# Optimization experiments

Measured on AMD Instinct MI355X. Metric: run time of the kernel, lower is better.

Reference implementation:

```python
import jax, jax.numpy as jnp
import numpy as np

NUM_HEADS = 16

def setup_inputs() -> dict:
    key = jax.random.key(0)
    k_x, k_wq, k_bq, k_wo, k_bo = jax.random.split(key, 5)
    B, S, D = 4, 2048, 1024
    x = jax.random.normal(k_x, (B, S, D), dtype=jnp.float32)
    # Flax Dense default init: lecun_normal for kernel, zeros for bias; use small normals here.
    w_qkv = jax.random.normal(k_wq, (D, 3 * D), dtype=jnp.float32) * (D ** -0.5)
    b_qkv = jnp.zeros((3 * D,), dtype=jnp.float32)
    w_out = jax.random.normal(k_wo, (D, D), dtype=jnp.float32) * (D ** -0.5)
    b_out = jnp.zeros((D,), dtype=jnp.float32)
    return {"x": x, "w_qkv": w_qkv, "b_qkv": b_qkv, "w_out": w_out, "b_out": b_out}

def reference(x, w_qkv, b_qkv, w_out, b_out):
    B, S, D = x.shape
    H = NUM_HEADS
    hd = D // H
    scale = hd ** -0.5
    qkv = x @ w_qkv + b_qkv                                  # [B,S,3D]
    qkv = qkv.reshape(B, S, 3, H, hd)
    qkv = jnp.transpose(qkv, (2, 0, 3, 1, 4))                # [3,B,H,S,hd]
    q, k, v = qkv[0], qkv[1], qkv[2]
    attn = jnp.einsum("bhqd,bhkd->bhqk", q, k) * scale       # [B,H,S,S]
    attn = jax.nn.softmax(attn, axis=-1)
    out = jnp.einsum("bhqk,bhkd->bhqd", attn, v)             # [B,H,S,hd]
    out = jnp.transpose(out, (0, 2, 1, 3)).reshape(B, S, D)
    return out @ w_out + b_out
```

## Files before the change

### kernel.cpp

```cpp
#include <hip/hip_runtime.h>
#include <cstdint>
#include <cstddef>

#define B_    4
#define S_    2048
#define D_    1024
#define H_    16
#define HD_   64
#define M_    8192
#define NQKV  3072

typedef __bf16 bf16;
typedef __bf16 bf16x4 __attribute__((ext_vector_type(4)));
typedef __bf16 bf16x8 __attribute__((ext_vector_type(8)));
typedef float  f32x2  __attribute__((ext_vector_type(2)));
typedef float  f32x4  __attribute__((ext_vector_type(4)));
typedef float  f32x16 __attribute__((ext_vector_type(16)));
typedef uint32_t u32x2 __attribute__((ext_vector_type(2)));
typedef uint32_t u32x4 __attribute__((ext_vector_type(4)));

#define MFMA16(a, b, c) __builtin_amdgcn_mfma_f32_16x16x32_bf16(a, b, c, 0, 0, 0)

__device__ __forceinline__ void gl2lds16(const void* g, void* l) {
  __builtin_amdgcn_global_load_lds(
      (__attribute__((address_space(1))) void*)(uintptr_t)g,
      (__attribute__((address_space(3))) void*)l, 16, 0, 0);
}

__device__ __forceinline__ uint32_t pkbf16(float a, float b) {
  union { bf16 h[2]; uint32_t u; } z;
  z.h[0] = (bf16)a; z.h[1] = (bf16)b;
  return z.u;
}

__global__ __launch_bounds__(256) void cast_f32_bf16(const float* __restrict__ in,
                                                     bf16* __restrict__ out, int n4) {
  int i = blockIdx.x * 256 + threadIdx.x;
  if (i >= n4) return;
  float4 v = ((const float4*)in)[i];
  bf16x4 o;
  o[0] = (bf16)v.x; o[1] = (bf16)v.y; o[2] = (bf16)v.z; o[3] = (bf16)v.w;
  ((bf16x4*)out)[i] = o;
}

__global__ __launch_bounds__(256) void transpose_cast(const float* __restrict__ in,
                                                      bf16* __restrict__ out, int R, int C) {
  __shared__ float tile[32][33];
  int bx = blockIdx.x * 32, by = blockIdx.y * 32;
  int tx = threadIdx.x, ty = threadIdx.y;
#pragma unroll
  for (int i = 0; i < 32; i += 8)
    tile[ty + i][tx] = in[(size_t)(by + ty + i) * C + bx + tx];
  __syncthreads();
#pragma unroll
  for (int i = 0; i < 32; i += 8)
    out[(size_t)(bx + ty + i) * R + by + tx] = (bf16)tile[tx][ty + i];
}

template <bool OUT_BF16>
__global__ __launch_bounds__(512, 2) void gemm256(const bf16* __restrict__ A,
                                                  const bf16* __restrict__ Bt,
                                                  const float* __restrict__ bias,
                                                  void* __restrict__ Cptr,
                                                  int M, int N, int K) {
  extern __shared__ __align__(16) bf16 sm[];
  const int tid  = threadIdx.x;
  const int lane = tid & 63, w = tid >> 6;
  const int lo   = lane & 15, quad = lane >> 4;
  const int wr   = w >> 1, wc = w & 1;
  const int xcd  = blockIdx.x & 7, g = blockIdx.x >> 3;
  const int mi_  = g & 3, n_ = g >> 2;
  const int bm   = (xcd * 4 + mi_) * 256, bn = n_ * 128;

  const bf16* Ag = A  + (size_t)bm * K;
  const bf16* Bg = Bt + (size_t)bn * K;

  const int swzl  = lo & 7;
  const int laneA = (wr * 64 + lo) * 64;
  const int laneB = (wc * 64 + lo) * 64;
  const int pc0   = (quad ^ swzl) * 8;
  const int pc1   = ((4 + quad) ^ swzl) * 8;

  int aoffG[4], boffG[2];
#pragma unroll
  for (int la = 0; la < 4; ++la) {
    int ca = la * 512 + tid, row = ca >> 3, s = ca & 7;
    aoffG[la] = row * K + ((s ^ (row & 7)) * 8);
  }
#pragma unroll
  for (int lb = 0; lb < 2; ++lb) {
    int cb = lb * 512 + tid, row = cb >> 3, s = cb & 7;
    boffG[lb] = row * K + ((s ^ (row & 7)) * 8);
  }
  const int T = K >> 6;

  f32x4 acc[4][4];
  const f32x4 zero = {0.f, 0.f, 0.f, 0.f};
#pragma unroll
  for (int i = 0; i < 4; ++i)
#pragma unroll
    for (int j = 0; j < 4; ++j) acc[i][j] = zero;

#pragma unroll
  for (int la = 0; la < 4; ++la)
    gl2lds16(Ag + aoffG[la], sm + (la * 512 + tid) * 8);
#pragma unroll
  for (int lb = 0; lb < 2; ++lb)
    gl2lds16(Bg + boffG[lb], sm + 16384 + (lb * 512 + tid) * 8);
#pragma unroll
  for (int la = 0; la < 4; ++la)
    gl2lds16(Ag + 64 + aoffG[la], sm + 24576 + (la * 512 + tid) * 8);
#pragma unroll
  for (int lb = 0; lb < 2; ++lb)
    gl2lds16(Bg + 64 + boffG[lb], sm + 24576 + 16384 + (lb * 512 + tid) * 8);
  asm volatile("s_waitcnt vmcnt(6)" ::: "memory");
  __builtin_amdgcn_s_barrier();

  auto body = [&](int t, bool st) __attribute__((always_inline)) {
    bf16* As_ = sm + (t % 3) * 24576;
    bf16* Bs_ = As_ + 16384;
    bf16* An_ = sm + ((t + 2) % 3) * 24576;
    bf16* Bn_ = An_ + 16384;
    const size_t kg = (size_t)(t + 2) * 64;
    bf16x8 av0, av1, bv[4];

    av0 = *(const bf16x8*)&As_[laneA + 0 * 1024 + pc0];
    av1 = *(const bf16x8*)&As_[laneA + 1 * 1024 + pc0];
#pragma unroll
    for (int j = 0; j < 4; ++j)
      bv[j] = *(const bf16x8*)&Bs_[laneB + j * 1024 + pc0];
    if (st) {
      gl2lds16(Ag + kg + aoffG[0], An_ + (0 * 512 + tid) * 8);
      gl2lds16(Ag + kg + aoffG[1], An_ + (1 * 512 + tid) * 8);
    }
    __builtin_amdgcn_s_barrier();
    __builtin_amdgcn_s_setprio(1);
#pragma unroll
    for (int j = 0; j < 4; ++j) {
      acc[0][j] = MFMA16(av0, bv[j], acc[0][j]);
      acc[1][j] = MFMA16(av1, bv[j], acc[1][j]);
    }
    __builtin_amdgcn_s_setprio(0);

    av0 = *(const bf16x8*)&As_[laneA + 2 * 1024 + pc0];
    av1 = *(const bf16x8*)&As_[laneA + 3 * 1024 + pc0];
    if (st) {
      gl2lds16(Ag + kg + aoffG[2], An_ + (2 * 512 + tid) * 8);
      gl2lds16(Ag + kg + aoffG[3], An_ + (3 * 512 + tid) * 8);
    }
    __builtin_amdgcn_s_barrier();
    __builtin_amdgcn_s_setprio(1);
#pragma unroll
    for (int j = 0; j < 4; ++j) {
      acc[2][j] = MFMA16(av0, bv[j], acc[2][j]);
      acc[3][j] = MFMA16(av1, bv[j], acc[3][j]);
    }
    __builtin_amdgcn_s_setprio(0);

    av0 = *(const bf16x8*)&As_[laneA + 0 * 1024 + pc1];
    av1 = *(const bf16x8*)&As_[laneA + 1 * 1024 + pc1];
#pragma unroll
    for (int j = 0; j < 4; ++j)
      bv[j] = *(const bf16x8*)&Bs_[laneB + j * 1024 + pc1];
    if (st)
      gl2lds16(Bg + kg + boffG[0], Bn_ + (0 * 512 + tid) * 8);
    __builtin_amdgcn_s_barrier();
    __builtin_amdgcn_s_setprio(1);
#pragma unroll
    for (int j = 0; j < 4; ++j) {
      acc[0][j] = MFMA16(av0, bv[j], acc[0][j]);
      acc[1][j] = MFMA16(av1, bv[j], acc[1][j]);
    }
    __builtin_amdgcn_s_setprio(0);

    av0 = *(const bf16x8*)&As_[laneA + 2 * 1024 + pc1];
    av1 = *(const bf16x8*)&As_[laneA + 3 * 1024 + pc1];
    if (st)
      gl2lds16(Bg + kg + boffG[1], Bn_ + (1 * 512 + tid) * 8);
    __builtin_amdgcn_s_barrier();
    __builtin_amdgcn_s_setprio(1);
#pragma unroll
    for (int j = 0; j < 4; ++j) {
      acc[2][j] = MFMA16(av0, bv[j], acc[2][j]);
      acc[3][j] = MFMA16(av1, bv[j], acc[3][j]);
    }
    __builtin_amdgcn_s_setprio(0);
  };

#pragma unroll 1
  for (int t = 0; t < T - 2; ++t) {
    body(t, true);
    asm volatile("s_waitcnt vmcnt(6)" ::: "memory");
    __builtin_amdgcn_s_barrier();
  }
  body(T - 2, false);
  asm volatile("s_waitcnt vmcnt(0)" ::: "memory");
  __builtin_amdgcn_s_barrier();
  body(T - 1, false);

#pragma unroll
  for (int j = 0; j < 4; ++j) {
    int cg = bn + wc * 64 + j * 16 + lo;
    float bsv = bias[cg];
#pragma unroll
    for (int i = 0; i < 4; ++i) {
      int rg = bm + wr * 64 + i * 16 + quad * 4;
#pragma unroll
      for (int r = 0; r < 4; ++r) {
        float v = acc[i][j][r] + bsv;
        if (OUT_BF16) ((bf16*)Cptr)[(size_t)(rg + r) * N + cg] = (bf16)v;
        else          ((float*)Cptr)[(size_t)(rg + r) * N + cg] = v;
      }
    }
  }
}

__global__ __launch_bounds__(256, 2) void flash_attn(const bf16* __restrict__ qkv,
                                                     bf16* __restrict__ out) {
  __shared__ __align__(16) bf16 smem[16384];
  bf16* const Ksm = smem;
  bf16* const Vsm = smem + 8192;

  const int tid  = threadIdx.x;
  const int lane = tid & 63, wq = tid >> 6;
  const int l31  = lane & 31;
  const int e    = lane >> 5;
  const int hi8  = e * 8, hi4 = e * 4;

  const int bid = blockIdx.x;
  const int qb  = bid >> 6;
  const int bh  = bid & 63;
  const int h   = bh & 15;
  const int b   = bh >> 4;
  const int q0  = qb * 256;
  const size_t rowb = (size_t)b * S_;
  const bf16* qbase = qkv + rowb * NQKV + h * HD_;
  const bf16* kbase = qbase + D_;
  const bf16* vbase = qbase + 2 * D_;

  bf16x8 qfA[4], qfB[4];
  {
    const bf16* qrow0 = qbase + (size_t)(q0 + wq * 64 + l31) * NQKV;
    const bf16* qrow1 = qrow0 + (size_t)32 * NQKV;
#pragma unroll
    for (int c = 0; c < 4; ++c) {
      qfA[c] = *(const bf16x8*)(qrow0 + c * 16 + hi8);
      qfB[c] = *(const bf16x8*)(qrow1 + c * 16 + hi8);
    }
  }

  int kq_off[2];
#pragma unroll
  for (int it = 0; it < 2; ++it) {
    int ci = it * 256 + tid;
    int s  = ci >> 3;
    int x  = (ci & 7) ^ (s & 7);
    kq_off[it] = s * NQKV + x * 8;
  }
  int vs_d[2], vs_s[2], vs_off[2];
#pragma unroll
  for (int u = 0; u < 2; ++u) {
    int idx = u * 256 + tid;
    int d0 = (idx & 31) * 2;
    int s0 = (idx >> 5) * 4;
    vs_d[u] = d0;
    vs_s[u] = s0;
    vs_off[u] = (((s0 >> 3) ^ ((d0 >> 1) & 7)) * 8) + (s0 & 7);
  }

  uint32_t vreg[2][4];

  const f32x16 zero16 = {0.f,0.f,0.f,0.f,0.f,0.f,0.f,0.f,0.f,0.f,0.f,0.f,0.f,0.f,0.f,0.f};
  f32x16 oacc[2][2];
  oacc[0][0] = zero16; oacc[0][1] = zero16;
  oacc[1][0] = zero16; oacc[1][1] = zero16;
  f32x16 sAc[2], sBc[2];
  f32x2 psA = {0.f, 0.f}, psB = {0.f, 0.f};
  const float c2 = 0.125f * 1.44269504088896341f;

#define KDMA(KT, PB) {                                                      \
    const bf16* kb_ = kbase + (size_t)(KT) * 64 * NQKV;                     \
    _Pragma("unroll")                                                       \
    for (int it = 0; it < 2; ++it)                                          \
      gl2lds16(kb_ + kq_off[it], Ksm + (PB) * 4096 + (it * 256 + wq * 64) * 8); \
  }
#define VLOAD(KT) {                                                         \
    const bf16* vb_ = vbase + (size_t)(KT) * 64 * NQKV;                     \
    _Pragma("unroll")                                                       \
    for (int u = 0; u < 2; ++u)                                             \
      _Pragma("unroll")                                                     \
      for (int j = 0; j < 4; ++j)                                           \
        vreg[u][j] = *(const uint32_t*)(vb_ + (size_t)(vs_s[u] + j) * NQKV + vs_d[u]); \
  }
#define VWRITE(PB) {                                                        \
    _Pragma("unroll")                                                       \
    for (int u = 0; u < 2; ++u) {                                           \
      int d0_ = vs_d[u];                                                    \
      uint32_t lo0 = __builtin_amdgcn_perm(vreg[u][1], vreg[u][0], 0x05040100u); \
      uint32_t lo1 = __builtin_amdgcn_perm(vreg[u][3], vreg[u][2], 0x05040100u); \
      uint32_t hi0 = __builtin_amdgcn_perm(vreg[u][1], vreg[u][0], 0x07060302u); \
      uint32_t hi1 = __builtin_amdgcn_perm(vreg[u][3], vreg[u][2], 0x07060302u); \
      u32x2 lov = {lo0, lo1}, hiv = {hi0, hi1};                             \
      *(u32x2*)&Vsm[(PB) * 4096 + (d0_ + 0) * 64 + vs_off[u]] = lov;        \
      *(u32x2*)&Vsm[(PB) * 4096 + (d0_ + 1) * 64 + vs_off[u]] = hiv;        \
    }                                                                       \
  }

  auto smfma = [&](int P) __attribute__((always_inline)) {
    sAc[0] = zero16; sBc[0] = zero16;
    sAc[1] = zero16; sBc[1] = zero16;
    __builtin_amdgcn_s_setprio(1);
#pragma unroll
    for (int c = 0; c < 4; ++c) {
#pragma unroll
      for (int kk = 0; kk < 2; ++kk) {
        int srow = kk * 32 + l31;
        int swz  = (srow & 7) * 8;
        bf16x8 kf = *(const bf16x8*)&Ksm[P * 4096 + srow * 64 + ((c * 16 + hi8) ^ swz)];
        sAc[kk] = __builtin_amdgcn_mfma_f32_32x32x16_bf16(kf, qfA[c], sAc[kk], 0, 0, 0);
        sBc[kk] = __builtin_amdgcn_mfma_f32_32x32x16_bf16(kf, qfB[c], sBc[kk], 0, 0, 0);
      }
    }
    __builtin_amdgcn_s_setprio(0);
  };

  auto softpv = [&](int P) __attribute__((always_inline)) {
#pragma unroll
    for (int kk = 0; kk < 2; ++kk) {
      uint32_t Q8a[8], Q8b[8];
#pragma unroll
      for (int i = 0; i < 8; ++i) {
        f32x2 sva, svb;
        sva[0] = sAc[kk][2 * i]; sva[1] = sAc[kk][2 * i + 1];
        svb[0] = sBc[kk][2 * i]; svb[1] = sBc[kk][2 * i + 1];
        f32x2 ta = sva * c2 - 16.0f;
        f32x2 tb = svb * c2 - 16.0f;
        float a0 = __builtin_amdgcn_exp2f(ta[0]);
        float a1 = __builtin_amdgcn_exp2f(ta[1]);
        float b0 = __builtin_amdgcn_exp2f(tb[0]);
        float b1 = __builtin_amdgcn_exp2f(tb[1]);
        psA += (f32x2){a0, a1};
        psB += (f32x2){b0, b1};
        Q8a[i] = pkbf16(a0, a1);
        Q8b[i] = pkbf16(b0, b1);
      }
#pragma unroll
      for (int mh = 0; mh < 2; ++mh) {
        const int m = kk * 2 + mh, bq = mh * 4;
        u32x4 pda, pdb;
#if __has_builtin(__builtin_amdgcn_permlane32_swap)
        u32x2 wa0 = __builtin_amdgcn_permlane32_swap(Q8a[bq],     Q8a[bq + 2], false, false);
        u32x2 wa1 = __builtin_amdgcn_permlane32_swap(Q8a[bq + 1], Q8a[bq + 3], false, false);
        pda[0] = wa0[0]; pda[1] = wa1[0]; pda[2] = wa0[1]; pda[3] = wa1[1];
        u32x2 wb0 = __builtin_amdgcn_permlane32_swap(Q8b[bq],     Q8b[bq + 2], false, false);
        u32x2 wb1 = __builtin_amdgcn_permlane32_swap(Q8b[bq + 1], Q8b[bq + 3], false, false);
        pdb[0] = wb0[0]; pdb[1] = wb1[0]; pdb[2] = wb0[1]; pdb[3] = wb1[1];
#else
        {
          uint32_t s0 = e ? Q8a[bq]     : Q8a[bq + 2];
          uint32_t s1 = e ? Q8a[bq + 1] : Q8a[bq + 3];
          uint32_t r0 = __shfl_xor(s0, 32);
          uint32_t r1 = __shfl_xor(s1, 32);
          pda[0] = e ? r0 : Q8a[bq];
          pda[1] = e ? r1 : Q8a[bq + 1];
          pda[2] = e ? Q8a[bq + 2] : r0;
          pda[3] = e ? Q8a[bq + 3] : r1;
        }
        {
          uint32_t s0 = e ? Q8b[bq]     : Q8b[bq + 2];
          uint32_t s1 = e ? Q8b[bq + 1] : Q8b[bq + 3];
          uint32_t r0 = __shfl_xor(s0, 32);
          uint32_t r1 = __shfl_xor(s1, 32);
          pdb[0] = e ? r0 : Q8b[bq];
          pdb[1] = e ? r1 : Q8b[bq + 1];
          pdb[2] = e ? Q8b[bq + 2] : r0;
          pdb[3] = e ? Q8b[bq + 3] : r1;
        }
#endif
        bf16x8 pfa = __builtin_bit_cast(bf16x8, pda);
        bf16x8 pfb = __builtin_bit_cast(bf16x8, pdb);
        __builtin_amdgcn_s_setprio(1);
#pragma unroll
        for (int dt = 0; dt < 2; ++dt) {
          int drow = dt * 32 + l31;
          int swv  = (drow >> 1) & 7;
          bf16x8 vf = *(const bf16x8*)&Vsm[P * 4096 + drow * 64 + (((m * 2 + e) ^ swv) * 8)];
          oacc[dt][0] = __builtin_amdgcn_mfma_f32_32x32x16_bf16(vf, pfa, oacc[dt][0], 0, 0, 0);
          oacc[dt][1] = __builtin_amdgcn_mfma_f32_32x32x16_bf16(vf, pfb, oacc[dt][1], 0, 0, 0);
        }
        __builtin_amdgcn_s_setprio(0);
      }
    }
  };

  KDMA(0, 0);
  VLOAD(0);
  VWRITE(0);
  VLOAD(1);
  __syncthreads();
  smfma(0);

#pragma unroll 1
  for (int kt = 0; kt < 31; ++kt) {
    const int buf = kt & 1;
    KDMA(kt + 1, buf ^ 1);
    VWRITE(buf ^ 1);
    {
      int kn2 = (kt + 2 < 32) ? kt + 2 : 31;
      VLOAD(kn2);
    }
    softpv(buf);
    __syncthreads();
    smfma(buf ^ 1);
  }
  softpv(1);

#undef KDMA
#undef VLOAD
#undef VWRITE

  float lsumA = psA[0] + psA[1];
  float lsumB = psB[0] + psB[1];
  lsumA += __shfl_xor(lsumA, 32);
  lsumB += __shfl_xor(lsumB, 32);

  __syncthreads();
  bf16* Os = smem;
  {
    float invA = 1.f / lsumA;
    float invB = 1.f / lsumB;
#pragma unroll
    for (int qs = 0; qs < 2; ++qs) {
      float inv = qs ? invB : invA;
      int ql = wq * 64 + qs * 32 + l31;
      int swO = (ql >> 1) & 7;
#pragma unroll
      for (int dt = 0; dt < 2; ++dt) {
#pragma unroll
        for (int g = 0; g < 4; ++g) {
          bf16x4 ov;
#pragma unroll
          for (int jj = 0; jj < 4; ++jj)
            ov[jj] = (bf16)(oacc[dt][qs][g * 4 + jj] * inv);
          *(bf16x4*)&Os[ql * 64 + (((dt * 4 + g) ^ swO) * 8) + hi4] = ov;
        }
      }
    }
  }
  __syncthreads();
#pragma unroll
  for (int it = 0; it < 8; ++it) {
    int idx = it * 256 + tid;
    int row = idx >> 3, c8 = idx & 7;
    bf16x8 t = *(const bf16x8*)&Os[row * 64 + ((c8 ^ ((row >> 1) & 7)) * 8)];
    *(bf16x8*)&out[(rowb + q0 + row) * D_ + h * HD_ + c8 * 8] = t;
  }
}

extern "C" void kernel_launch(void* const* d_in, const int* in_sizes, int n_in,
                              void* d_out, int out_size, void* d_ws, size_t ws_size,
                              hipStream_t stream) {
  const float* x     = (const float*)d_in[0];
  const float* w_qkv = (const float*)d_in[1];
  const float* b_qkv = (const float*)d_in[2];
  const float* w_out = (const float*)d_in[3];
  const float* b_out = (const float*)d_in[4];
  float* out = (float*)d_out;

  char* ws = (char*)d_ws;
  bf16* xb    = (bf16*)(ws);
  bf16* wqkvT = (bf16*)(ws + (size_t)16777216);
  bf16* woutT = (bf16*)(ws + (size_t)23068672);
  bf16* qkvb  = (bf16*)(ws + (size_t)25165824);
  bf16* attnb = (bf16*)(ws + (size_t)75497472);

  static int attr_done = 0;
  if (!attr_done) {
    hipFuncSetAttribute(reinterpret_cast<const void*>(&gemm256<true>),
                        hipFuncAttributeMaxDynamicSharedMemorySize, 147456);
    hipFuncSetAttribute(reinterpret_cast<const void*>(&gemm256<false>),
                        hipFuncAttributeMaxDynamicSharedMemorySize, 147456);
    attr_done = 1;
  }

  cast_f32_bf16<<<(M_ * D_ / 4 + 255) / 256, 256, 0, stream>>>(x, xb, M_ * D_ / 4);
  transpose_cast<<<dim3(NQKV / 32, D_ / 32), dim3(32, 8), 0, stream>>>(w_qkv, wqkvT, D_, NQKV);
  transpose_cast<<<dim3(D_ / 32, D_ / 32), dim3(32, 8), 0, stream>>>(w_out, woutT, D_, D_);

  gemm256<true><<<(M_ / 256) * (NQKV / 128), 512, 147456, stream>>>(
      xb, wqkvT, b_qkv, (void*)qkvb, M_, NQKV, D_);

  flash_attn<<<B_ * H_ * (S_ / 256), 256, 0, stream>>>(qkvb, attnb);

  gemm256<false><<<(M_ / 256) * (D_ / 128), 512, 147456, stream>>>(
      attnb, woutT, b_out, (void*)out, M_, D_, D_);
}
```

Before: 277.1 us.

## Triple-buffer K in LDS and interleave QK^T MFMA with softmax-PV halves

K tiles move to a three-slot LDS ring and are prefetched two tiles ahead. The S-accumulator registers are double-buffered, so the QK^T MFMAs for the next tile are interleaved half-by-half with the softmax and PV work of the current tile. The loop is unrolled by two to swap register sets. The goal is to overlap exp/permute VALU work with MFMA and hide K load latency, at the cost of more LDS (40KB) and about 128 extra VGPRs of accumulators, which may hurt occupancy or cause spills under launch_bounds(256,2).

```diff
diff --git a/kernel.cpp b/kernel.cpp
--- a/kernel.cpp
+++ b/kernel.cpp
@@ -217,9 +217,9 @@
 
 __global__ __launch_bounds__(256, 2) void flash_attn(const bf16* __restrict__ qkv,
                                                      bf16* __restrict__ out) {
-  __shared__ __align__(16) bf16 smem[16384];
+  __shared__ __align__(16) bf16 smem[20480];
   bf16* const Ksm = smem;
-  bf16* const Vsm = smem + 8192;
+  bf16* const Vsm = smem + 12288;
 
   const int tid  = threadIdx.x;
   const int lane = tid & 63, wq = tid >> 6;
@@ -274,15 +274,15 @@
   f32x16 oacc[2][2];
   oacc[0][0] = zero16; oacc[0][1] = zero16;
   oacc[1][0] = zero16; oacc[1][1] = zero16;
-  f32x16 sAc[2], sBc[2];
+  f32x16 s0A0, s0B0, s0A1, s0B1, s1A0, s1B0, s1A1, s1B1;
   f32x2 psA = {0.f, 0.f}, psB = {0.f, 0.f};
   const float c2 = 0.125f * 1.44269504088896341f;
 
-#define KDMA(KT, PB) {                                                      \
+#define KDMA(KT, SLOT) {                                                    \
     const bf16* kb_ = kbase + (size_t)(KT) * 64 * NQKV;                     \
     _Pragma("unroll")                                                       \
     for (int it = 0; it < 2; ++it)                                          \
-      gl2lds16(kb_ + kq_off[it], Ksm + (PB) * 4096 + (it * 256 + wq * 64) * 8); \
+      gl2lds16(kb_ + kq_off[it], Ksm + (SLOT) * 4096 + (it * 256 + wq * 64) * 8); \
   }
 #define VLOAD(KT) {                                                         \
     const bf16* vb_ = vbase + (size_t)(KT) * 64 * NQKV;                     \
@@ -305,119 +305,116 @@
       *(u32x2*)&Vsm[(PB) * 4096 + (d0_ + 1) * 64 + vs_off[u]] = hiv;        \
     }                                                                       \
   }
-
-  auto smfma = [&](int P) __attribute__((always_inline)) {
-    sAc[0] = zero16; sBc[0] = zero16;
-    sAc[1] = zero16; sBc[1] = zero16;
-    __builtin_amdgcn_s_setprio(1);
-#pragma unroll
-    for (int c = 0; c < 4; ++c) {
-#pragma unroll
-      for (int kk = 0; kk < 2; ++kk) {
-        int srow = kk * 32 + l31;
-        int swz  = (srow & 7) * 8;
-        bf16x8 kf = *(const bf16x8*)&Ksm[P * 4096 + srow * 64 + ((c * 16 + hi8) ^ swz)];
-        sAc[kk] = __builtin_amdgcn_mfma_f32_32x32x16_bf16(kf, qfA[c], sAc[kk], 0, 0, 0);
-        sBc[kk] = __builtin_amdgcn_mfma_f32_32x32x16_bf16(kf, qfB[c], sBc[kk], 0, 0, 0);
-      }
-    }
-    __builtin_amdgcn_s_setprio(0);
-  };
-
-  auto softpv = [&](int P) __attribute__((always_inline)) {
-#pragma unroll
-    for (int kk = 0; kk < 2; ++kk) {
-      uint32_t Q8a[8], Q8b[8];
-#pragma unroll
-      for (int i = 0; i < 8; ++i) {
-        f32x2 sva, svb;
-        sva[0] = sAc[kk][2 * i]; sva[1] = sAc[kk][2 * i + 1];
-        svb[0] = sBc[kk][2 * i]; svb[1] = sBc[kk][2 * i + 1];
-        f32x2 ta = sva * c2 - 16.0f;
-        f32x2 tb = svb * c2 - 16.0f;
-        float a0 = __builtin_amdgcn_exp2f(ta[0]);
-        float a1 = __builtin_amdgcn_exp2f(ta[1]);
-        float b0 = __builtin_amdgcn_exp2f(tb[0]);
-        float b1 = __builtin_amdgcn_exp2f(tb[1]);
-        psA += (f32x2){a0, a1};
-        psB += (f32x2){b0, b1};
-        Q8a[i] = pkbf16(a0, a1);
-        Q8b[i] = pkbf16(b0, b1);
-      }
-#pragma unroll
-      for (int mh = 0; mh < 2; ++mh) {
-        const int m = kk * 2 + mh, bq = mh * 4;
-        u32x4 pda, pdb;
+#define SMFMA_H(KK, SLOT, SA, SB) {                                         \
+    f32x16 sa_ = zero16, sb_ = zero16;                                      \
+    int srow_ = (KK) * 32 + l31;                                            \
+    int swz_  = (srow_ & 7) * 8;                                            \
+    __builtin_amdgcn_s_setprio(1);                                          \
+    _Pragma("unroll")                                                       \
+    for (int c = 0; c < 4; ++c) {                                           \
+      bf16x8 kf_ = *(const bf16x8*)&Ksm[(SLOT) * 4096 + srow_ * 64 + ((c * 16 + hi8) ^ swz_)]; \
+      sa_ = __builtin_amdgcn_mfma_f32_32x32x16_bf16(kf_, qfA[c], sa_, 0, 0, 0); \
+      sb_ = __builtin_amdgcn_mfma_f32_32x32x16_bf16(kf_, qfB[c], sb_, 0, 0, 0); \
+    }                                                                       \
+    __builtin_amdgcn_s_setprio(0);                                          \
+    SA = sa_; SB = sb_;                                                     \
+  }
 #if __has_builtin(__builtin_amdgcn_permlane32_swap)
-        u32x2 wa0 = __builtin_amdgcn_permlane32_swap(Q8a[bq],     Q8a[bq + 2], false, false);
-        u32x2 wa1 = __builtin_amdgcn_permlane32_swap(Q8a[bq + 1], Q8a[bq + 3], false, false);
-        pda[0] = wa0[0]; pda[1] = wa1[0]; pda[2] = wa0[1]; pda[3] = wa1[1];
-        u32x2 wb0 = __builtin_amdgcn_permlane32_swap(Q8b[bq],     Q8b[bq + 2], false, false);
-        u32x2 wb1 = __builtin_amdgcn_permlane32_swap(Q8b[bq + 1], Q8b[bq + 3], false, false);
-        pdb[0] = wb0[0]; pdb[1] = wb1[0]; pdb[2] = wb0[1]; pdb[3] = wb1[1];
+#define RELAY(Q8, PD, BQ) {                                                 \
+    u32x2 w0_ = __builtin_amdgcn_permlane32_swap(Q8[BQ],     Q8[(BQ) + 2], false, false); \
+    u32x2 w1_ = __builtin_amdgcn_permlane32_swap(Q8[(BQ) + 1], Q8[(BQ) + 3], false, false); \
+    PD[0] = w0_[0]; PD[1] = w1_[0]; PD[2] = w0_[1]; PD[3] = w1_[1];         \
+  }
 #else
-        {
-          uint32_t s0 = e ? Q8a[bq]     : Q8a[bq + 2];
-          uint32_t s1 = e ? Q8a[bq + 1] : Q8a[bq + 3];
-          uint32_t r0 = __shfl_xor(s0, 32);
-          uint32_t r1 = __shfl_xor(s1, 32);
-          pda[0] = e ? r0 : Q8a[bq];
-          pda[1] = e ? r1 : Q8a[bq + 1];
-          pda[2] = e ? Q8a[bq + 2] : r0;
-          pda[3] = e ? Q8a[bq + 3] : r1;
-        }
-        {
-          uint32_t s0 = e ? Q8b[bq]     : Q8b[bq + 2];
-          uint32_t s1 = e ? Q8b[bq + 1] : Q8b[bq + 3];
-          uint32_t r0 = __shfl_xor(s0, 32);
-          uint32_t r1 = __shfl_xor(s1, 32);
-          pdb[0] = e ? r0 : Q8b[bq];
-          pdb[1] = e ? r1 : Q8b[bq + 1];
-          pdb[2] = e ? Q8b[bq + 2] : r0;
-          pdb[3] = e ? Q8b[bq + 3] : r1;
-        }
+#define RELAY(Q8, PD, BQ) {                                                 \
+    uint32_t s0_ = e ? Q8[BQ]       : Q8[(BQ) + 2];                         \
+    uint32_t s1_ = e ? Q8[(BQ) + 1] : Q8[(BQ) + 3];                         \
+    uint32_t r0_ = __shfl_xor(s0_, 32);                                     \
+    uint32_t r1_ = __shfl_xor(s1_, 32);                                     \
+    PD[0] = e ? r0_ : Q8[BQ];                                               \
+    PD[1] = e ? r1_ : Q8[(BQ) + 1];                                         \
+    PD[2] = e ? Q8[(BQ) + 2] : r0_;                                         \
+    PD[3] = e ? Q8[(BQ) + 3] : r1_;                                         \
+  }
 #endif
-        bf16x8 pfa = __builtin_bit_cast(bf16x8, pda);
-        bf16x8 pfb = __builtin_bit_cast(bf16x8, pdb);
-        __builtin_amdgcn_s_setprio(1);
-#pragma unroll
-        for (int dt = 0; dt < 2; ++dt) {
-          int drow = dt * 32 + l31;
-          int swv  = (drow >> 1) & 7;
-          bf16x8 vf = *(const bf16x8*)&Vsm[P * 4096 + drow * 64 + (((m * 2 + e) ^ swv) * 8)];
-          oacc[dt][0] = __builtin_amdgcn_mfma_f32_32x32x16_bf16(vf, pfa, oacc[dt][0], 0, 0, 0);
-          oacc[dt][1] = __builtin_amdgcn_mfma_f32_32x32x16_bf16(vf, pfb, oacc[dt][1], 0, 0, 0);
-        }
-        __builtin_amdgcn_s_setprio(0);
-      }
-    }
-  };
+#define SOFTPV_H(KK, PB, SA, SB) {                                          \
+    uint32_t Q8a_[8], Q8b_[8];                                              \
+    _Pragma("unroll")                                                       \
+    for (int i = 0; i < 8; ++i) {                                           \
+      f32x2 sva_, svb_;                                                     \
+      sva_[0] = SA[2 * i]; sva_[1] = SA[2 * i + 1];                         \
+      svb_[0] = SB[2 * i]; svb_[1] = SB[2 * i + 1];                         \
+      f32x2 ta_ = sva_ * c2 - 16.0f;                                        \
+      f32x2 tb_ = svb_ * c2 - 16.0f;                                        \
+      float a0_ = __builtin_amdgcn_exp2f(ta_[0]);                           \
+      float a1_ = __builtin_amdgcn_exp2f(ta_[1]);                           \
+      float b0_ = __builtin_amdgcn_exp2f(tb_[0]);                           \
+      float b1_ = __builtin_amdgcn_exp2f(tb_[1]);                           \
+      psA += (f32x2){a0_, a1_};                                             \
+      psB += (f32x2){b0_, b1_};                                             \
+      Q8a_[i] = pkbf16(a0_, a1_);                                           \
+      Q8b_[i] = pkbf16(b0_, b1_);                                           \
+    }                                                                       \
+    _Pragma("unroll")                                                       \
+    for (int mh = 0; mh < 2; ++mh) {                                        \
+      const int m_ = (KK) * 2 + mh, bq_ = mh * 4;                           \
+      u32x4 pda_, pdb_;                                                     \
+      RELAY(Q8a_, pda_, bq_);                                               \
+      RELAY(Q8b_, pdb_, bq_);                                               \
+      bf16x8 pfa_ = __builtin_bit_cast(bf16x8, pda_);                       \
+      bf16x8 pfb_ = __builtin_bit_cast(bf16x8, pdb_);                       \
+      __builtin_amdgcn_s_setprio(1);                                        \
+      _Pragma("unroll")                                                     \
+      for (int dt = 0; dt < 2; ++dt) {                                      \
+        int drow_ = dt * 32 + l31;                                          \
+        int swv_  = (drow_ >> 1) & 7;                                       \
+        bf16x8 vf_ = *(const bf16x8*)&Vsm[(PB) * 4096 + drow_ * 64 + (((m_ * 2 + e) ^ swv_) * 8)]; \
+        oacc[dt][0] = __builtin_amdgcn_mfma_f32_32x32x16_bf16(vf_, pfa_, oacc[dt][0], 0, 0, 0); \
+        oacc[dt][1] = __builtin_amdgcn_mfma_f32_32x32x16_bf16(vf_, pfb_, oacc[dt][1], 0, 0, 0); \
+      }                                                                     \
+      __builtin_amdgcn_s_setprio(0);                                        \
+    }                                                                       \
+  }
+#define BODY(KT, CA0, CB0, CA1, CB1, NA0, NB0, NA1, NB1) {                  \
+    const int buf_ = (KT) & 1;                                              \
+    const int sl2_ = ((KT) + 2) % 3;                                        \
+    const int sl1_ = ((KT) + 1) % 3;                                        \
+    int kn2_ = ((KT) + 2 < 32) ? (KT) + 2 : 31;                             \
+    KDMA(kn2_, sl2_);                                                       \
+    VWRITE(buf_ ^ 1);                                   \
+    VLOAD(kn2_);                                                            \
+    SOFTPV_H(0, buf_, CA0, CB0);                                            \
+    SMFMA_H(0, sl1_, NA0, NB0);                                             \
+    SOFTPV_H(1, buf_, CA1, CB1);                                            \
+    SMFMA_H(1, sl1_, NA1, NB1);                                             \
+    __syncthreads();                                                        \
+  }
 
   KDMA(0, 0);
+  KDMA(1, 1);
   VLOAD(0);
   VWRITE(0);
   VLOAD(1);
   __syncthreads();
-  smfma(0);
+  SMFMA_H(0, 0, s0A0, s0B0);
+  SMFMA_H(1, 0, s0A1, s0B1);
 
 #pragma unroll 1
-  for (int kt = 0; kt < 31; ++kt) {
-    const int buf = kt & 1;
-    KDMA(kt + 1, buf ^ 1);
-    VWRITE(buf ^ 1);
-    {
-      int kn2 = (kt + 2 < 32) ? kt + 2 : 31;
-      VLOAD(kn2);
-    }
-    softpv(buf);
-    __syncthreads();
-    smfma(buf ^ 1);
-  }
-  softpv(1);
-
+  for (int t2 = 0; t2 < 15; ++t2) {
+    BODY(2 * t2,     s0A0, s0B0, s0A1, s0B1, s1A0, s1B0, s1A1, s1B1);
+    BODY(2 * t2 + 1, s1A0, s1B0, s1A1, s1B1, s0A0, s0B0, s0A1, s0B1);
+  }
+  BODY(30, s0A0, s0B0, s0A1, s0B1, s1A0, s1B0, s1A1, s1B1);
+  SOFTPV_H(0, 1, s1A0, s1B0);
+  SOFTPV_H(1, 1, s1A1, s1B1);
+
+#undef BODY
+#undef SOFTPV_H
+#undef RELAY
+#undef SMFMA_H
+#undef VWRITE
+#undef VLOAD
 #undef KDMA
-#undef VLOAD
-#undef VWRITE
 
   float lsumA = psA[0] + psA[1];
   float lsumB = psB[0] + psB[1];
```

Result: faster. 270.4 us (-2.4%).
